# Optimization experiments

Measured on AMD Instinct MI355X. Metric: run time of the kernel, lower is better.

## Reference

```python
import jax, jax.numpy as jnp
import numpy as np

N = 100000   # nodes
E = 600000   # edges
H = 128      # hidden_size
G = 4000     # graphs in batch
T = 128      # num_tasks
ATOM_DIMS = np.array([119, 5, 12, 12, 10, 6, 6, 2, 2])  # OGB atom feature vocab sizes
OFFSETS = jnp.asarray(np.concatenate([[0], np.cumsum(ATOM_DIMS)[:-1]]), dtype=jnp.int64)


def setup_inputs() -> dict:
    key = jax.random.key(0)
    ks = jax.random.split(key, 12)
    x = jax.random.randint(ks[0], (N, 9), 0, 2)
    edge_index = jax.random.randint(ks[1], (2, E), 0, N)
    batch = jnp.sort(jax.random.randint(ks[2], (N,), 0, G))
    s = 1.0 / np.sqrt(H)
    atom_emb = jax.random.normal(ks[3], (int(ATOM_DIMS.sum()), H), dtype=jnp.float32) * 0.02
    W1 = jax.random.normal(ks[4], (H, H), dtype=jnp.float32) * s
    b1 = jnp.zeros((H,), dtype=jnp.float32)
    W2 = jax.random.normal(ks[5], (H, H), dtype=jnp.float32) * s
    b2 = jnp.zeros((H,), dtype=jnp.float32)
    W3 = jax.random.normal(ks[6], (H, H), dtype=jnp.float32) * s
    b3 = jnp.zeros((H,), dtype=jnp.float32)
    Wl = jax.random.normal(ks[7], (H, T), dtype=jnp.float32) * s
    bl = jnp.zeros((T,), dtype=jnp.float32)
    return dict(x=x, edge_index=edge_index, batch=batch, atom_emb=atom_emb,
                W1=W1, b1=b1, W2=W2, b2=b2, W3=W3, b3=b3, Wl=Wl, bl=bl)


def _gcn_conv(h, W, b, src, dst, dinv):
    # GCNConv: linear transform, then symmetric-normalized scatter-add with self-loops
    h = h @ W                                        # [N,H]
    norm = dinv[src] * dinv[dst]                     # [E]
    msg = h[src] * norm[:, None]                     # [E,H]
    agg = jax.ops.segment_sum(msg, dst, num_segments=N)
    # self-loop contribution: norm_ii = dinv_i^2, weight 1
    return agg + (dinv * dinv)[:, None] * h + b


def reference(x, edge_index, batch, atom_emb, W1, b1, W2, b2, W3, b3, Wl, bl):
    src, dst = edge_index[0], edge_index[1]
    # degree with self-loops (edge_weight = 1)
    deg = jax.ops.segment_sum(jnp.ones((E,), dtype=atom_emb.dtype), dst, num_segments=N) + 1.0
    dinv = jax.lax.rsqrt(deg)
    # AtomEncoder: sum of per-feature embeddings (one concatenated table + offsets)
    h = atom_emb[x + OFFSETS[None, :]].sum(axis=1)   # [N,H]
    h = jax.nn.relu(_gcn_conv(h, W1, b1, src, dst, dinv))
    h = jax.nn.relu(_gcn_conv(h, W2, b2, src, dst, dinv))
    h = _gcn_conv(h, W3, b3, src, dst, dinv)
    # global mean pool over graphs
    cnt = jax.ops.segment_sum(jnp.ones((N,), dtype=h.dtype), batch, num_segments=G)
    pooled = jax.ops.segment_sum(h, batch, num_segments=G) / jnp.maximum(cnt, 1.0)[:, None]
    return pooled @ Wl + bl                          # [G,T]
```

## Files before the change

### kernel.cpp

```cpp
#include <hip/hip_runtime.h>

#define NN 100000
#define EE 600000
#define HH 128
#define GG 4000
#define TT 128
#define PAD 64

typedef short short8 __attribute__((ext_vector_type(8)));
typedef unsigned short ushort8v __attribute__((ext_vector_type(8)));
typedef float floatx4 __attribute__((ext_vector_type(4)));

static __device__ __forceinline__ float bf2f(unsigned short u) {
  union { unsigned int i; float f; } v; v.i = ((unsigned int)u) << 16; return v.f;
}
static __device__ __forceinline__ unsigned short f2bf(float f) {
  union { float f; unsigned int i; } v; v.f = f;
  unsigned int r = (v.i + 0x7FFFu + ((v.i >> 16) & 1u)) >> 16;
  return (unsigned short)r;
}

#define DB ((EE / 4 + 255) / 256)
#define NB ((NN + 255) / 256)

__global__ __launch_bounds__(256) void fill_enc_wt_k(const int* __restrict__ ei,
                                                     int* __restrict__ cnt,
                                                     int* __restrict__ csr_pad,
                                                     const int* __restrict__ x,
                                                     const float* __restrict__ emb,
                                                     unsigned short* __restrict__ h0,
                                                     const float* __restrict__ W1,
                                                     const float* __restrict__ W2,
                                                     const float* __restrict__ W3,
                                                     unsigned short* __restrict__ Wt) {
  if (blockIdx.x < DB) {
    int e4 = (blockIdx.x * 256 + threadIdx.x) * 4;
    if (e4 >= EE) return;
    int4 s = *(const int4*)(ei + e4);
    int4 d = *(const int4*)(ei + EE + e4);
    int o0 = atomicAdd(&cnt[d.x], 1);
    int o1 = atomicAdd(&cnt[d.y], 1);
    int o2 = atomicAdd(&cnt[d.z], 1);
    int o3 = atomicAdd(&cnt[d.w], 1);
    if (o0 < PAD) csr_pad[d.x * PAD + o0] = s.x;
    if (o1 < PAD) csr_pad[d.y * PAD + o1] = s.y;
    if (o2 < PAD) csr_pad[d.z * PAD + o2] = s.z;
    if (o3 < PAD) csr_pad[d.w * PAD + o3] = s.w;
  } else if (blockIdx.x < DB + NN / 16) {
    const int lane = threadIdx.x & 63;
    const int wid  = threadIdx.x >> 6;
    const int l16  = lane & 15;
    const int n = (blockIdx.x - DB) * 16 + wid * 4 + (lane >> 4);
    const int off[9] = {0, 119, 124, 136, 148, 158, 164, 170, 172};
    int xv = (l16 < 9) ? x[n * 9 + l16] : 0;
    float s[8] = {0.f, 0.f, 0.f, 0.f, 0.f, 0.f, 0.f, 0.f};
#pragma unroll
    for (int f = 0; f < 9; f++) {
      int idx = __shfl(xv, (lane & 48) | f, 64) + off[f];
      const float* ep = emb + (size_t)idx * HH + l16 * 8;
      float4 e0 = *(const float4*)ep;
      float4 e1 = *(const float4*)(ep + 4);
      s[0] += e0.x; s[1] += e0.y; s[2] += e0.z; s[3] += e0.w;
      s[4] += e1.x; s[5] += e1.y; s[6] += e1.z; s[7] += e1.w;
    }
    ushort8v o;
#pragma unroll
    for (int j = 0; j < 8; j++) o[j] = f2bf(s[j]);
    *(ushort8v*)(h0 + (size_t)n * HH + l16 * 8) = o;
  } else {
    int f = (blockIdx.x - DB - NN / 16) * 256 + threadIdx.x;
    int wsel = f >> 14;
    int r = (f >> 7) & 127;
    int k = f & 127;
    const float* W = (wsel == 0) ? W1 : (wsel == 1) ? W2 : W3;
    Wt[wsel * HH * HH + r * HH + k] = f2bf(W[k * HH + r]);
  }
}

__global__ __launch_bounds__(256) void dinv_gs_k(const int* __restrict__ cnt,
                                                 float* __restrict__ dinv,
                                                 const int* __restrict__ batch,
                                                 int* __restrict__ gs) {
  const int i = blockIdx.x * 256 + threadIdx.x;
  if (i < NN) {
    dinv[i] = rsqrtf((float)cnt[i] + 1.0f);
    int b0 = batch[i];
    int b1 = (i + 1 < NN) ? batch[i + 1] : GG;
    for (int g = b0 + 1; g <= b1; g++) gs[g] = i + 1;
    if (i == 0)
      for (int g = 0; g <= b0; g++) gs[g] = 0;
  }
}

template <bool L1GATHER>
__global__ __launch_bounds__(256) void agg_bf_k(const int* __restrict__ deg,
                                                const int* __restrict__ csr_pad,
                                                const unsigned short* __restrict__ Hs,
                                                const float* __restrict__ dinv,
                                                unsigned short* __restrict__ Aggs) {
  const int lane = threadIdx.x & 63;
  const int wid  = threadIdx.x >> 6;
  const int l16  = lane & 15;
  const int n = blockIdx.x * 16 + wid * 4 + (lane >> 4);
  const int beg = n * PAD;
  const int end = beg + deg[n];
  const int last = end - 1;
  const float dn = dinv[n];
  float acc[8];
  {
    ushort8v v = *(const ushort8v*)(Hs + (size_t)n * HH + l16 * 8);
    const float sw = L1GATHER ? dn : 1.0f;
#pragma unroll
    for (int j = 0; j < 8; j++) acc[j] = sw * bf2f(v[j]);
  }
  int i = beg;
  if (i < end) {
    int c0 = csr_pad[i];
    int c1 = csr_pad[min(i + 1, last)];
    int c2 = csr_pad[min(i + 2, last)];
    int c3 = csr_pad[min(i + 3, last)];
    while (true) {
      float m0 = 1.f;
      float m1 = (i + 1 < end) ? 1.f : 0.f;
      float m2 = (i + 2 < end) ? 1.f : 0.f;
      float m3 = (i + 3 < end) ? 1.f : 0.f;
      if (L1GATHER) {
        m0 *= dinv[c0]; m1 *= dinv[c1]; m2 *= dinv[c2]; m3 *= dinv[c3];
      }
      ushort8v v0 = *(const ushort8v*)(Hs + (size_t)c0 * HH + l16 * 8);
      ushort8v v1 = *(const ushort8v*)(Hs + (size_t)c1 * HH + l16 * 8);
      ushort8v v2 = *(const ushort8v*)(Hs + (size_t)c2 * HH + l16 * 8);
      ushort8v v3 = *(const ushort8v*)(Hs + (size_t)c3 * HH + l16 * 8);
      const int ni = i + 4;
      int p0 = c0, p1 = c1, p2 = c2, p3 = c3;
      if (ni < end) {
        p0 = csr_pad[ni];
        p1 = csr_pad[min(ni + 1, last)];
        p2 = csr_pad[min(ni + 2, last)];
        p3 = csr_pad[min(ni + 3, last)];
      }
      if (L1GATHER) {
#pragma unroll
        for (int j = 0; j < 8; j++)
          acc[j] += m0 * bf2f(v0[j]) + m1 * bf2f(v1[j]) + m2 * bf2f(v2[j]) + m3 * bf2f(v3[j]);
      } else {
#pragma unroll
        for (int j = 0; j < 8; j++)
          acc[j] += bf2f(v0[j]) + m1 * bf2f(v1[j]) + m2 * bf2f(v2[j]) + m3 * bf2f(v3[j]);
      }
      i = ni;
      if (i >= end) break;
      c0 = p0; c1 = p1; c2 = p2; c3 = p3;
    }
  }
  ushort8v o;
#pragma unroll
  for (int j = 0; j < 8; j++) o[j] = f2bf(dn * acc[j]);
  *(ushort8v*)(Aggs + (size_t)n * HH + l16 * 8) = o;
}

template <bool LAST>
__global__ __launch_bounds__(256) void gemm_mfma_k(const unsigned short* __restrict__ A,
                                                   const unsigned short* __restrict__ Wt,
                                                   const float* __restrict__ b,
                                                   const float* __restrict__ dinv,
                                                   unsigned short* __restrict__ Out) {
  const int w = threadIdx.x >> 6;
  const int l = threadIdx.x & 63;
  const int m16 = l & 15;
  const int q8  = (l >> 4) * 8;
  const int bm  = blockIdx.x * 128 + w * 32;

  floatx4 acc[2][8];
#pragma unroll
  for (int i = 0; i < 2; i++)
#pragma unroll
    for (int j = 0; j < 8; j++) acc[i][j] = (floatx4){0.f, 0.f, 0.f, 0.f};

  for (int q = 0; q < 4; q++) {
    const int k0 = q * 32;
    short8 a[2];
#pragma unroll
    for (int ti = 0; ti < 2; ti++) {
      int row = bm + ti * 16 + m16;
      a[ti] = (row < NN) ? *(const short8*)(A + (size_t)row * HH + k0 + q8)
                         : (short8){0, 0, 0, 0, 0, 0, 0, 0};
    }
#pragma unroll
    for (int tn = 0; tn < 8; tn++) {
      short8 bf = *(const short8*)(Wt + (size_t)(tn * 16 + m16) * HH + k0 + q8);
      acc[0][tn] = __builtin_amdgcn_mfma_f32_16x16x32_bf16(a[0], bf, acc[0][tn], 0, 0, 0);
      acc[1][tn] = __builtin_amdgcn_mfma_f32_16x16x32_bf16(a[1], bf, acc[1][tn], 0, 0, 0);
    }
  }

  float bias[8];
#pragma unroll
  for (int tn = 0; tn < 8; tn++) bias[tn] = b[tn * 16 + m16];

#pragma unroll
  for (int ti = 0; ti < 2; ti++) {
    const int rbase = bm + ti * 16 + (l >> 4) * 4;
#pragma unroll
    for (int r = 0; r < 4; r++) {
      const int row = rbase + r;
      if (row < NN) {
        const float dv = LAST ? 1.0f : dinv[row];
#pragma unroll
        for (int tn = 0; tn < 8; tn++) {
          const int col = tn * 16 + m16;
          float v = acc[ti][tn][r] + bias[tn];
          if (!LAST) v = dv * fmaxf(v, 0.f);
          Out[(size_t)row * HH + col] = f2bf(v);
        }
      }
    }
  }
}

__global__ __launch_bounds__(128) void pool_final_k(const int* __restrict__ gs,
                                                    const unsigned short* __restrict__ h3,
                                                    const float* __restrict__ Wl,
                                                    const float* __restrict__ bl,
                                                    float* __restrict__ out) {
  const int g = blockIdx.x;
  const int t = threadIdx.x;
  const int beg = gs[g];
  const int end = gs[g + 1];
  float s = 0.f;
  for (int n = beg; n < end; n++) s += bf2f(h3[(size_t)n * HH + t]);
  __shared__ float p[128];
  p[t] = s / (float)max(end - beg, 1);
  __syncthreads();
  float acc = bl[t];
#pragma unroll 8
  for (int h = 0; h < HH; h++) acc += p[h] * Wl[h * TT + t];
  out[(size_t)g * TT + t] = acc;
}

extern "C" void kernel_launch(void* const* d_in, const int* in_sizes, int n_in,
                              void* d_out, int out_size, void* d_ws, size_t ws_size,
                              hipStream_t stream) {
  const int*   x     = (const int*)d_in[0];
  const int*   ei    = (const int*)d_in[1];
  const int*   batch = (const int*)d_in[2];
  const float* emb   = (const float*)d_in[3];
  const float* W1    = (const float*)d_in[4];
  const float* b1    = (const float*)d_in[5];
  const float* W2    = (const float*)d_in[6];
  const float* b2    = (const float*)d_in[7];
  const float* W3    = (const float*)d_in[8];
  const float* b3    = (const float*)d_in[9];
  const float* Wl    = (const float*)d_in[10];
  const float* bl    = (const float*)d_in[11];
  float* out = (float*)d_out;

  unsigned short* bufA = (unsigned short*)d_ws;
  unsigned short* bufB = bufA + (size_t)NN * HH;
  unsigned short* Wt   = bufB + (size_t)NN * HH;
  float* dinv   = (float*)(Wt + 3 * HH * HH);
  int*   cnt    = (int*)(dinv + NN);
  int*   gs     = cnt + NN;
  int*   csr    = gs + GG + 1;

  hipMemsetAsync(cnt, 0, NN * sizeof(int), stream);

  fill_enc_wt_k<<<DB + NN / 16 + 192, 256, 0, stream>>>(ei, cnt, csr,
                                                        x, emb, bufA,
                                                        W1, W2, W3, Wt);
  dinv_gs_k<<<NB, 256, 0, stream>>>(cnt, dinv, batch, gs);

  const int gemm_grid = (NN + 127) / 128;
  const int agg_grid  = NN / 16;

  agg_bf_k<true><<<agg_grid, 256, 0, stream>>>(cnt, csr, bufA, dinv, bufB);
  gemm_mfma_k<false><<<gemm_grid, 256, 0, stream>>>(bufB, Wt, b1, dinv, bufA);

  agg_bf_k<false><<<agg_grid, 256, 0, stream>>>(cnt, csr, bufA, dinv, bufB);
  gemm_mfma_k<false><<<gemm_grid, 256, 0, stream>>>(bufB, Wt + HH * HH, b2, dinv, bufA);

  agg_bf_k<false><<<agg_grid, 256, 0, stream>>>(cnt, csr, bufA, dinv, bufB);
  gemm_mfma_k<true><<<gemm_grid, 256, 0, stream>>>(bufB, Wt + 2 * HH * HH, b3, dinv, bufA);

  pool_final_k<<<GG, 128, 0, stream>>>(gs, bufA, Wl, bl, out);
}
```

Baseline: 317.1 us.

## Drop dinv kernel, recompute rsqrt from counts, fold graph-start scan into aggregation

Removes the separate dinv/graph-start kernel. The normalization is recomputed inline from the degree counts with rsqrt in both the aggregation and GEMM kernels. The graph-start computation moves into extra blocks appended to the first aggregation launch. The aggregation gather loop is also widened from 4 to 8 neighbors per iteration for more memory-level parallelism, at the cost of more registers and more wasted masked loads for low-degree nodes.

After: 315.8 us. Within noise of the previous version (-0.4%).

```diff
diff --git a/kernel.cpp b/kernel.cpp
--- a/kernel.cpp
+++ b/kernel.cpp
@@ -22,6 +22,7 @@
 
 #define DB ((EE / 4 + 255) / 256)
 #define NB ((NN + 255) / 256)
+#define AGG_GRID (NN / 16)
 
 __global__ __launch_bounds__(256) void fill_enc_wt_k(const int* __restrict__ ei,
                                                      int* __restrict__ cnt,
@@ -77,35 +78,33 @@
   }
 }
 
-__global__ __launch_bounds__(256) void dinv_gs_k(const int* __restrict__ cnt,
-                                                 float* __restrict__ dinv,
-                                                 const int* __restrict__ batch,
-                                                 int* __restrict__ gs) {
-  const int i = blockIdx.x * 256 + threadIdx.x;
-  if (i < NN) {
-    dinv[i] = rsqrtf((float)cnt[i] + 1.0f);
-    int b0 = batch[i];
-    int b1 = (i + 1 < NN) ? batch[i + 1] : GG;
-    for (int g = b0 + 1; g <= b1; g++) gs[g] = i + 1;
-    if (i == 0)
-      for (int g = 0; g <= b0; g++) gs[g] = 0;
-  }
-}
-
 template <bool L1GATHER>
-__global__ __launch_bounds__(256) void agg_bf_k(const int* __restrict__ deg,
+__global__ __launch_bounds__(256) void agg_bf_k(const int* __restrict__ cnt,
                                                 const int* __restrict__ csr_pad,
                                                 const unsigned short* __restrict__ Hs,
-                                                const float* __restrict__ dinv,
-                                                unsigned short* __restrict__ Aggs) {
+                                                unsigned short* __restrict__ Aggs,
+                                                const int* __restrict__ batch,
+                                                int* __restrict__ gs) {
+  if (L1GATHER && blockIdx.x >= AGG_GRID) {
+    const int i = (blockIdx.x - AGG_GRID) * 256 + threadIdx.x;
+    if (i < NN) {
+      int b0 = batch[i];
+      int b1 = (i + 1 < NN) ? batch[i + 1] : GG;
+      for (int g = b0 + 1; g <= b1; g++) gs[g] = i + 1;
+      if (i == 0)
+        for (int g = 0; g <= b0; g++) gs[g] = 0;
+    }
+    return;
+  }
   const int lane = threadIdx.x & 63;
   const int wid  = threadIdx.x >> 6;
   const int l16  = lane & 15;
   const int n = blockIdx.x * 16 + wid * 4 + (lane >> 4);
+  const int deg = cnt[n];
   const int beg = n * PAD;
-  const int end = beg + deg[n];
+  const int end = beg + deg;
   const int last = end - 1;
-  const float dn = dinv[n];
+  const float dn = rsqrtf((float)deg + 1.0f);
   float acc[8];
   {
     ushort8v v = *(const ushort8v*)(Hs + (size_t)n * HH + l16 * 8);
@@ -115,42 +114,36 @@
   }
   int i = beg;
   if (i < end) {
-    int c0 = csr_pad[i];
-    int c1 = csr_pad[min(i + 1, last)];
-    int c2 = csr_pad[min(i + 2, last)];
-    int c3 = csr_pad[min(i + 3, last)];
+    int c[8];
+#pragma unroll
+    for (int j = 0; j < 8; j++) c[j] = csr_pad[min(i + j, last)];
     while (true) {
-      float m0 = 1.f;
-      float m1 = (i + 1 < end) ? 1.f : 0.f;
-      float m2 = (i + 2 < end) ? 1.f : 0.f;
-      float m3 = (i + 3 < end) ? 1.f : 0.f;
+      float m[8];
+      m[0] = 1.f;
+#pragma unroll
+      for (int j = 1; j < 8; j++) m[j] = (i + j < end) ? 1.f : 0.f;
       if (L1GATHER) {
-        m0 *= dinv[c0]; m1 *= dinv[c1]; m2 *= dinv[c2]; m3 *= dinv[c3];
+#pragma unroll
+        for (int j = 0; j < 8; j++) m[j] *= rsqrtf((float)cnt[c[j]] + 1.0f);
       }
-      ushort8v v0 = *(const ushort8v*)(Hs + (size_t)c0 * HH + l16 * 8);
-      ushort8v v1 = *(const ushort8v*)(Hs + (size_t)c1 * HH + l16 * 8);
-      ushort8v v2 = *(const ushort8v*)(Hs + (size_t)c2 * HH + l16 * 8);
-      ushort8v v3 = *(const ushort8v*)(Hs + (size_t)c3 * HH + l16 * 8);
-      const int ni = i + 4;
-      int p0 = c0, p1 = c1, p2 = c2, p3 = c3;
+      ushort8v v[8];
+#pragma unroll
+      for (int j = 0; j < 8; j++)
+        v[j] = *(const ushort8v*)(Hs + (size_t)c[j] * HH + l16 * 8);
+      const int ni = i + 8;
+      int p[8];
       if (ni < end) {
-        p0 = csr_pad[ni];
-        p1 = csr_pad[min(ni + 1, last)];
-        p2 = csr_pad[min(ni + 2, last)];
-        p3 = csr_pad[min(ni + 3, last)];
+#pragma unroll
+        for (int j = 0; j < 8; j++) p[j] = csr_pad[min(ni + j, last)];
       }
-      if (L1GATHER) {
-#pragma unroll
-        for (int j = 0; j < 8; j++)
-          acc[j] += m0 * bf2f(v0[j]) + m1 * bf2f(v1[j]) + m2 * bf2f(v2[j]) + m3 * bf2f(v3[j]);
-      } else {
-#pragma unroll
-        for (int j = 0; j < 8; j++)
-          acc[j] += bf2f(v0[j]) + m1 * bf2f(v1[j]) + m2 * bf2f(v2[j]) + m3 * bf2f(v3[j]);
-      }
+#pragma unroll
+      for (int j = 0; j < 8; j++)
+#pragma unroll
+        for (int k = 0; k < 8; k++) acc[k] += m[j] * bf2f(v[j][k]);
       i = ni;
       if (i >= end) break;
-      c0 = p0; c1 = p1; c2 = p2; c3 = p3;
+#pragma unroll
+      for (int j = 0; j < 8; j++) c[j] = p[j];
     }
   }
   ushort8v o;
@@ -163,7 +156,7 @@
 __global__ __launch_bounds__(256) void gemm_mfma_k(const unsigned short* __restrict__ A,
                                                    const unsigned short* __restrict__ Wt,
                                                    const float* __restrict__ b,
-                                                   const float* __restrict__ dinv,
+                                                   const int* __restrict__ cnt,
                                                    unsigned short* __restrict__ Out) {
   const int w = threadIdx.x >> 6;
   const int l = threadIdx.x & 63;
@@ -205,7 +198,7 @@
     for (int r = 0; r < 4; r++) {
       const int row = rbase + r;
       if (row < NN) {
-        const float dv = LAST ? 1.0f : dinv[row];
+        const float dv = LAST ? 1.0f : rsqrtf((float)cnt[row] + 1.0f);
 #pragma unroll
         for (int tn = 0; tn < 8; tn++) {
           const int col = tn * 16 + m16;
@@ -258,8 +251,7 @@
   unsigned short* bufA = (unsigned short*)d_ws;
   unsigned short* bufB = bufA + (size_t)NN * HH;
   unsigned short* Wt   = bufB + (size_t)NN * HH;
-  float* dinv   = (float*)(Wt + 3 * HH * HH);
-  int*   cnt    = (int*)(dinv + NN);
+  int*   cnt    = (int*)(Wt + 3 * HH * HH);
   int*   gs     = cnt + NN;
   int*   csr    = gs + GG + 1;
 
@@ -268,19 +260,17 @@
   fill_enc_wt_k<<<DB + NN / 16 + 192, 256, 0, stream>>>(ei, cnt, csr,
                                                         x, emb, bufA,
                                                         W1, W2, W3, Wt);
-  dinv_gs_k<<<NB, 256, 0, stream>>>(cnt, dinv, batch, gs);
 
   const int gemm_grid = (NN + 127) / 128;
-  const int agg_grid  = NN / 16;
-
-  agg_bf_k<true><<<agg_grid, 256, 0, stream>>>(cnt, csr, bufA, dinv, bufB);
-  gemm_mfma_k<false><<<gemm_grid, 256, 0, stream>>>(bufB, Wt, b1, dinv, bufA);
-
-  agg_bf_k<false><<<agg_grid, 256, 0, stream>>>(cnt, csr, bufA, dinv, bufB);
-  gemm_mfma_k<false><<<gemm_grid, 256, 0, stream>>>(bufB, Wt + HH * HH, b2, dinv, bufA);
-
-  agg_bf_k<false><<<agg_grid, 256, 0, stream>>>(cnt, csr, bufA, dinv, bufB);
-  gemm_mfma_k<true><<<gemm_grid, 256, 0, stream>>>(bufB, Wt + 2 * HH * HH, b3, dinv, bufA);
+
+  agg_bf_k<true><<<AGG_GRID + NB, 256, 0, stream>>>(cnt, csr, bufA, bufB, batch, gs);
+  gemm_mfma_k<false><<<gemm_grid, 256, 0, stream>>>(bufB, Wt, b1, cnt, bufA);
+
+  agg_bf_k<false><<<AGG_GRID, 256, 0, stream>>>(cnt, csr, bufA, bufB, batch, gs);
+  gemm_mfma_k<false><<<gemm_grid, 256, 0, stream>>>(bufB, Wt + HH * HH, b2, cnt, bufA);
+
+  agg_bf_k<false><<<AGG_GRID, 256, 0, stream>>>(cnt, csr, bufA, bufB, batch, gs);
+  gemm_mfma_k<true><<<gemm_grid, 256, 0, stream>>>(bufB, Wt + 2 * HH * HH, b3, cnt, bufA);
 
   pool_final_k<<<GG, 128, 0, stream>>>(gs, bufA, Wl, bl, out);
 }
```
